# Kernel tuning notes

Hardware: AMD Instinct MI355X
Metric: run time of the kernel (lower is better)

The kernel has to match this reference:

```python
import jax, jax.numpy as jnp
import numpy as np

B = 524288   # batch of agents
N = 64       # neighbors (other agents)
H = 32       # hidden (hardcoded in original via zeros(1,32) and sqrt(32))
V = 256      # vocab_size
SCALE = np.float32(np.sqrt(32.0))  # original divides by sqrt(32) regardless of hidden


def setup_inputs() -> dict:
    key = jax.random.key(0)
    ks = jax.random.split(key, 24)
    lin = lambda k, i, o: (jax.random.normal(k, (i, o), jnp.float32) * (1.0 / np.sqrt(i)))
    inp = {
        'symbol': jax.random.randint(ks[0], (B,), 0, V, jnp.int32),
        'other_hidden': jax.random.normal(ks[1], (N, H), jnp.float32),
        'prev_hidden': jax.random.normal(ks[2], (B, H), jnp.float32),
        'emb': jax.random.normal(ks[3], (V, H), jnp.float32),
        'mem_gate': jnp.zeros((H,), jnp.float32),
        'Wm': lin(ks[4], H, H), 'bm': jnp.zeros((H,), jnp.float32),
        'Wq': lin(ks[5], H, H), 'bq': jnp.zeros((H,), jnp.float32),
        'Wk': lin(ks[6], H, H), 'bk': jnp.zeros((H,), jnp.float32),
        'Wv': lin(ks[7], H, H), 'bv': jnp.zeros((H,), jnp.float32),
        'W1': lin(ks[8], H, H), 'b1': jnp.zeros((H,), jnp.float32),
        'W2': lin(ks[9], H, H), 'b2': jnp.zeros((H,), jnp.float32),
        'W3': lin(ks[10], H, H), 'b3': jnp.zeros((H,), jnp.float32),
        'W4': lin(ks[11], H, H), 'b4': jnp.zeros((H,), jnp.float32),
        'Wa': lin(ks[12], H, 1), 'ba': jnp.zeros((1,), jnp.float32),
        'Ws': lin(ks[13], H, V), 'bs': jnp.zeros((V,), jnp.float32),
        'Wi': lin(ks[14], H, 3), 'bi': jnp.zeros((3,), jnp.float32),
    }
    return inp


def reference(symbol, other_hidden, prev_hidden, emb, mem_gate,
              Wm, bm, Wq, bq, Wk, bk, Wv, bv,
              W1, b1, W2, b2, W3, b3, W4, b4,
              Wa, ba, Ws, bs, Wi, bi):
    # embedding lookup
    h = emb[symbol]                                   # [B, H]
    # gated memory update
    gate = jax.nn.sigmoid(mem_gate)                   # [H]
    mem = jnp.tanh(prev_hidden @ Wm + bm)             # [B, H]
    h = h * (1.0 - gate) + mem * gate
    # social attention over shared neighbor set
    q = h @ Wq + bq                                   # [B, H]
    k = other_hidden @ Wk + bk                        # [N, H]
    v = other_hidden @ Wv + bv                        # [N, H]
    scores = (q @ k.T) / SCALE                        # [B, N]
    weights = jax.nn.softmax(scores, axis=-1)
    h = h + (weights @ v) * 0.3
    for W, b in ((W1, b1), (W2, b2), (W3, b3), (W4, b4)):
        h = h + jnp.tanh(h @ W + b) * 0.3
    # output heads
    action = jnp.tanh(h @ Wa + ba)                    # [B, 1]
    symbol_pred = h @ Ws + bs                         # [B, V]
    intent = h @ Wi + bi                              # [B, 3]
    return (action, symbol_pred, intent, h)
```

## Files before the change

kernel.cpp:

```cpp
#include <hip/hip_runtime.h>
#include <hip/hip_bf16.h>

constexpr int BTOT = 524288;
constexpr int NN   = 64;
constexpr int H    = 32;
constexpr int V    = 256;

typedef __attribute__((ext_vector_type(4))) float f32x4;
typedef __attribute__((ext_vector_type(4))) int   int4v;
typedef __attribute__((ext_vector_type(8))) short short8;

union FragU { int4v i; short8 s; };

__device__ __forceinline__ float fast_rcp(float x){ return __builtin_amdgcn_rcpf(x); }
__device__ __forceinline__ float fast_tanh(float x){
    float e = __expf(2.0f * x);
    return 1.0f - 2.0f * fast_rcp(e + 1.0f);
}
__device__ __forceinline__ int pkbf(float lo, float hi){
    union { __hip_bfloat162 h2; int i; } u;
    u.h2.x = __float2bfloat16(lo);
    u.h2.y = __float2bfloat16(hi);
    return u.i;
}
__device__ __forceinline__ void nt_store4(float* p, f32x4 v){
    __builtin_nontemporal_store(v, reinterpret_cast<f32x4*>(p));
}
__device__ __forceinline__ void nt_store1(float* p, float v){
    __builtin_nontemporal_store(v, p);
}

__device__ __attribute__((aligned(16))) int   g_Wfrag [6*2*64*4];
__device__ __attribute__((aligned(16))) int   g_Kfrag [4*64*4];
__device__ __attribute__((aligned(16))) int   g_Vfrag [2*2*64*4];
__device__ __attribute__((aligned(16))) int   g_Wsfrag[16*64*4];
__device__ __attribute__((aligned(16))) float g_biasd [6*64*8];
__device__ __attribute__((aligned(16))) float g_gated [64*8];
__device__ __attribute__((aligned(16))) float g_wad   [64*8];
__device__ __attribute__((aligned(16))) float g_wid   [64*24];

__global__ void precompute(const float* __restrict__ other_hidden,
                           const float* __restrict__ mem_gate,
                           const float* __restrict__ Wk, const float* __restrict__ bk,
                           const float* __restrict__ Wv, const float* __restrict__ bv,
                           const float* __restrict__ Wm, const float* __restrict__ bm,
                           const float* __restrict__ Wq, const float* __restrict__ bq,
                           const float* __restrict__ W1, const float* __restrict__ b1,
                           const float* __restrict__ W2, const float* __restrict__ b2,
                           const float* __restrict__ W3, const float* __restrict__ b3,
                           const float* __restrict__ W4, const float* __restrict__ b4,
                           const float* __restrict__ Wa, const float* __restrict__ Wi,
                           const float* __restrict__ Ws)
{
    __shared__ float Kst[64][32];
    __shared__ float Vst[64][32];
    __shared__ float gateS[32];
    const int t = threadIdx.x;

    if (t < 32) gateS[t] = fast_rcp(1.0f + __expf(-mem_gate[t]));
    {
        int n = t >> 2, c = (t & 3) * 8;
        float ak[8], av[8];
        #pragma unroll
        for (int i = 0; i < 8; ++i){ ak[i] = bk[c+i]; av[i] = bv[c+i]; }
        #pragma unroll
        for (int j = 0; j < H; ++j){
            float x = other_hidden[n*H + j];
            #pragma unroll
            for (int i = 0; i < 8; ++i){
                ak[i] = fmaf(x, Wk[j*H + c + i], ak[i]);
                av[i] = fmaf(x, Wv[j*H + c + i], av[i]);
            }
        }
        #pragma unroll
        for (int i = 0; i < 8; ++i){ Kst[n][c+i] = ak[i]; Vst[n][c+i] = av[i]; }
    }
    __syncthreads();

    #pragma unroll
    for (int w = 0; w < 6; ++w){
        const float* W = (w==0)?Wm : (w==1)?Wq : (w==2)?W1 : (w==3)?W2 : (w==4)?W3 : W4;
        for (int e = t; e < 128; e += 256){
            int mt = e >> 6, l = e & 63, la = l & 15, g = l >> 4;
            int m = mt*16 + la;
            int base = ((w*2 + mt)*64 + l)*4;
            #pragma unroll
            for (int j = 0; j < 4; ++j){
                int k0 = g*8 + 2*j;
                g_Wfrag[base + j] = pkbf(W[k0*H + m], W[(k0+1)*H + m]);
            }
        }
    }
    #pragma unroll
    for (int w = 0; w < 6; ++w){
        const float* bp_ = (w==0)?bm : (w==1)?bq : (w==2)?b1 : (w==3)?b2 : (w==4)?b3 : b4;
        for (int e = t; e < 512; e += 256){
            int l = e >> 3, idx = e & 7, mt = idx >> 2, r = idx & 3;
            int F = mt*16 + ((l>>4)&3)*4 + r;
            g_biasd[(w*64 + l)*8 + idx] = bp_[F];
        }
    }
    {
        int e = t;
        int mt = e >> 6, l = e & 63, la = l & 15, g = l >> 4;
        int n = mt*16 + la;
        #pragma unroll
        for (int j = 0; j < 4; ++j){
            int k0 = g*8 + 2*j;
            g_Kfrag[e*4 + j] = pkbf(Kst[n][k0], Kst[n][k0+1]);
        }
    }
    {
        int e = t;
        int mt = e >> 7, kt = (e >> 6) & 1, l = e & 63, la = l & 15, g = l >> 4;
        int m = mt*16 + la;
        #pragma unroll
        for (int j = 0; j < 4; ++j){
            int n0 = kt*32 + g*8 + 2*j;
            g_Vfrag[e*4 + j] = pkbf(Vst[n0][m], Vst[n0+1][m]);
        }
    }
    for (int e = t; e < 1024; e += 256){
        int mt = e >> 6, l = e & 63, la = l & 15, g = l >> 4;
        int m = mt*16 + la;
        #pragma unroll
        for (int j = 0; j < 4; ++j){
            int k0 = g*8 + 2*j;
            g_Wsfrag[e*4 + j] = pkbf(Ws[k0*V + m], Ws[(k0+1)*V + m]);
        }
    }
    for (int e = t; e < 512; e += 256){
        int l = e >> 3, idx = e & 7;
        int F = (idx>>2)*16 + ((l>>4)&3)*4 + (idx&3);
        g_gated[e] = gateS[F];
        g_wad[e]   = Wa[F];
    }
    for (int e = t; e < 1536; e += 256){
        int l = e / 24, m2 = e % 24, fidx = m2 / 3, j = m2 % 3;
        int F = (fidx>>2)*16 + ((l>>4)&3)*4 + (fidx&3);
        g_wid[e] = Wi[F*3 + j];
    }
}

__device__ __forceinline__ FragU d2b(f32x4 m0, f32x4 m1, int idxA, int idxB, bool glo){
    int p0a = pkbf(m0[0], m0[1]);
    int p1a = pkbf(m0[2], m0[3]);
    int p0b = pkbf(m1[0], m1[1]);
    int p1b = pkbf(m1[2], m1[3]);
    int tA0  = __builtin_amdgcn_ds_bpermute(idxA, p0a);
    int tA0b = __builtin_amdgcn_ds_bpermute(idxA, p0b);
    int tA1  = __builtin_amdgcn_ds_bpermute(idxA, p1a);
    int tA1b = __builtin_amdgcn_ds_bpermute(idxA, p1b);
    int tB0  = __builtin_amdgcn_ds_bpermute(idxB, p0a);
    int tB0b = __builtin_amdgcn_ds_bpermute(idxB, p0b);
    int tB1  = __builtin_amdgcn_ds_bpermute(idxB, p1a);
    int tB1b = __builtin_amdgcn_ds_bpermute(idxB, p1b);
    FragU r;
    r.i = int4v{ glo ? tA0 : tA0b, glo ? tA1 : tA1b,
                 glo ? tB0 : tB0b, glo ? tB1 : tB1b };
    return r;
}

__device__ __forceinline__ float bred_sum(float v, int bx16, int bx32){
    v += __int_as_float(__builtin_amdgcn_ds_bpermute(bx16, __float_as_int(v)));
    v += __int_as_float(__builtin_amdgcn_ds_bpermute(bx32, __float_as_int(v)));
    return v;
}
__device__ __forceinline__ float bred_max(float v, int bx16, int bx32){
    v = fmaxf(v, __int_as_float(__builtin_amdgcn_ds_bpermute(bx16, __float_as_int(v))));
    v = fmaxf(v, __int_as_float(__builtin_amdgcn_ds_bpermute(bx32, __float_as_int(v))));
    return v;
}
__device__ __forceinline__ f32x4 tanh4(f32x4 v){
    f32x4 r;
    r[0] = fast_tanh(v[0]); r[1] = fast_tanh(v[1]);
    r[2] = fast_tanh(v[2]); r[3] = fast_tanh(v[3]);
    return r;
}

#define MFMA(a, b, c) __builtin_amdgcn_mfma_f32_16x16x32_bf16((a), (b), (c), 0, 0, 0)

__global__ __launch_bounds__(256, 4) void social_main(
    const int*   __restrict__ symbol,
    const float* __restrict__ prev_hidden,
    const float* __restrict__ emb,
    const float* __restrict__ bs,
    const float* __restrict__ ba,
    const float* __restrict__ bi,
    float* __restrict__ out)
{
    const int tid = threadIdx.x;
    const int wv = tid >> 6, l = tid & 63;
    const int la = l & 15, g = l >> 4;
    const bool glo = (g < 2);
    const int idxA = (((g & 1) << 5) + la) << 2;
    const int idxB = idxA + 64;
    const int bx16 = (l ^ 16) << 2;
    const int bx32 = (l ^ 32) << 2;
    const int A0 = blockIdx.x * 128 + wv * 32;

    __shared__ f32x4 stgAll[4][256];
    __shared__ int4v sSF[1024];
    __shared__ float bsS[256];
    f32x4* buf = stgAll[wv];

    {
        const int4v* q4 = reinterpret_cast<const int4v*>(g_Wsfrag);
        for (int i = tid; i < 1024; i += 256) sSF[i] = q4[i];
        bsS[tid] = bs[tid];
    }
    __syncthreads();

    float* out_action = out;
    float* out_sym    = out + (size_t)BTOT;
    float* out_int    = out + (size_t)BTOT * (1 + V);
    float* out_h      = out + (size_t)BTOT * (1 + V + 3);

    const int4v* WF = reinterpret_cast<const int4v*>(g_Wfrag);
    const int4v* KF = reinterpret_cast<const int4v*>(g_Kfrag);
    const int4v* VF = reinterpret_cast<const int4v*>(g_Vfrag);
    const f32x4 zero4 = {0.f, 0.f, 0.f, 0.f};

    FragU phb[2];
    #pragma unroll
    for (int nt = 0; nt < 2; ++nt){
        const f32x4* p = reinterpret_cast<const f32x4*>(
            prev_hidden + (size_t)(A0 + nt*16 + la) * H + g*8);
        f32x4 v0 = p[0], v1 = p[1];
        phb[nt].i = int4v{ pkbf(v0[0],v0[1]), pkbf(v0[2],v0[3]),
                           pkbf(v1[0],v1[1]), pkbf(v1[2],v1[3]) };
    }

    f32x4 h_[2][2];
    {
        f32x4 bias[2];
        bias[0] = *reinterpret_cast<const f32x4*>(g_biasd + l*8);
        bias[1] = *reinterpret_cast<const f32x4*>(g_biasd + l*8 + 4);
        f32x4 m_[2][2];
        #pragma unroll
        for (int mt = 0; mt < 2; ++mt){
            FragU af; af.i = WF[(0*2 + mt)*64 + l];
            #pragma unroll
            for (int nt = 0; nt < 2; ++nt)
                m_[mt][nt] = MFMA(af.s, phb[nt].s, bias[mt]);
        }
        f32x4 gt[2];
        gt[0] = *reinterpret_cast<const f32x4*>(g_gated + l*8);
        gt[1] = *reinterpret_cast<const f32x4*>(g_gated + l*8 + 4);
        int sym0 = symbol[A0 + la], sym1 = symbol[A0 + 16 + la];
        #pragma unroll
        for (int mt = 0; mt < 2; ++mt)
        #pragma unroll
        for (int nt = 0; nt < 2; ++nt){
            const float* eb = emb + (size_t)(nt ? sym1 : sym0)*H + mt*16 + g*4;
            #pragma unroll
            for (int r = 0; r < 4; ++r){
                float gv = gt[mt][r];
                h_[mt][nt][r] = eb[r]*(1.0f - gv) + fast_tanh(m_[mt][nt][r])*gv;
            }
        }
    }

    f32x4 q_[2][2];
    {
        f32x4 bias[2];
        bias[0] = *reinterpret_cast<const f32x4*>(g_biasd + 512 + l*8);
        bias[1] = *reinterpret_cast<const f32x4*>(g_biasd + 512 + l*8 + 4);
        FragU hb[2] = { d2b(h_[0][0], h_[1][0], idxA, idxB, glo),
                        d2b(h_[0][1], h_[1][1], idxA, idxB, glo) };
        #pragma unroll
        for (int mt = 0; mt < 2; ++mt){
            FragU af; af.i = WF[(1*2 + mt)*64 + l];
            #pragma unroll
            for (int nt = 0; nt < 2; ++nt)
                q_[mt][nt] = MFMA(af.s, hb[nt].s, bias[mt]);
        }
    }

    f32x4 s_[4][2];
    {
        FragU qb[2] = { d2b(q_[0][0], q_[1][0], idxA, idxB, glo),
                        d2b(q_[0][1], q_[1][1], idxA, idxB, glo) };
        #pragma unroll
        for (int mt = 0; mt < 4; ++mt){
            FragU af; af.i = KF[mt*64 + l];
            #pragma unroll
            for (int nt = 0; nt < 2; ++nt)
                s_[mt][nt] = MFMA(af.s, qb[nt].s, zero4);
        }
    }

    const float INVS = 0.17677669529663687f;
    float coef[2];
    #pragma unroll
    for (int nt = 0; nt < 2; ++nt){
        float mx = s_[0][nt][0];
        #pragma unroll
        for (int mt = 0; mt < 4; ++mt)
        #pragma unroll
        for (int r = 0; r < 4; ++r) mx = fmaxf(mx, s_[mt][nt][r]);
        mx = bred_max(mx, bx16, bx32);
        float den = 0.f;
        #pragma unroll
        for (int mt = 0; mt < 4; ++mt)
        #pragma unroll
        for (int r = 0; r < 4; ++r){
            float w = __expf((s_[mt][nt][r] - mx) * INVS);
            s_[mt][nt][r] = w;
            den += w;
        }
        den = bred_sum(den, bx16, bx32);
        coef[nt] = 0.3f * fast_rcp(den);
    }

    {
        FragU wb[2][2];
        #pragma unroll
        for (int kt = 0; kt < 2; ++kt)
        #pragma unroll
        for (int nt = 0; nt < 2; ++nt)
            wb[kt][nt] = d2b(s_[2*kt][nt], s_[2*kt+1][nt], idxA, idxB, glo);
        #pragma unroll
        for (int mt = 0; mt < 2; ++mt){
            FragU vf0, vf1;
            vf0.i = VF[(mt*2 + 0)*64 + l];
            vf1.i = VF[(mt*2 + 1)*64 + l];
            #pragma unroll
            for (int nt = 0; nt < 2; ++nt){
                f32x4 acc = MFMA(vf0.s, wb[0][nt].s, zero4);
                acc = MFMA(vf1.s, wb[1][nt].s, acc);
                h_[mt][nt] += acc * coef[nt];
            }
        }
    }

    for (int blk = 0; blk < 4; ++blk){
        f32x4 bias[2];
        bias[0] = *reinterpret_cast<const f32x4*>(g_biasd + (2+blk)*512 + l*8);
        bias[1] = *reinterpret_cast<const f32x4*>(g_biasd + (2+blk)*512 + l*8 + 4);
        FragU hb[2] = { d2b(h_[0][0], h_[1][0], idxA, idxB, glo),
                        d2b(h_[0][1], h_[1][1], idxA, idxB, glo) };
        #pragma unroll
        for (int mt = 0; mt < 2; ++mt){
            FragU af; af.i = WF[((2+blk)*2 + mt)*64 + l];
            #pragma unroll
            for (int nt = 0; nt < 2; ++nt){
                f32x4 tv = MFMA(af.s, hb[nt].s, bias[mt]);
                h_[mt][nt] += 0.3f * tanh4(tv);
            }
        }
    }

    FragU hb[2] = { d2b(h_[0][0], h_[1][0], idxA, idxB, glo),
                    d2b(h_[0][1], h_[1][1], idxA, idxB, glo) };

    {
        union { f32x4 v[2]; float s[8]; } wa;
        wa.v[0] = *reinterpret_cast<const f32x4*>(g_wad + l*8);
        wa.v[1] = *reinterpret_cast<const f32x4*>(g_wad + l*8 + 4);
        float ba0 = ba[0];
        float act[2];
        #pragma unroll
        for (int nt = 0; nt < 2; ++nt){
            float acc = 0.f;
            #pragma unroll
            for (int mt = 0; mt < 2; ++mt)
            #pragma unroll
            for (int r = 0; r < 4; ++r)
                acc = fmaf(h_[mt][nt][r], wa.s[mt*4 + r], acc);
            acc = bred_sum(acc, bx16, bx32);
            act[nt] = fast_tanh(acc + ba0);
        }
        if (l < 16){
            nt_store1(out_action + A0 + la,      act[0]);
            nt_store1(out_action + A0 + 16 + la, act[1]);
        }
    }

    {
        union { f32x4 v[6]; float s[24]; } wi;
        #pragma unroll
        for (int k = 0; k < 6; ++k)
            wi.v[k] = *(reinterpret_cast<const f32x4*>(g_wid + l*24) + k);
        float bi0 = bi[0], bi1 = bi[1], bi2 = bi[2];
        #pragma unroll
        for (int nt = 0; nt < 2; ++nt){
            float i0 = 0.f, i1 = 0.f, i2 = 0.f;
            #pragma unroll
            for (int mt = 0; mt < 2; ++mt)
            #pragma unroll
            for (int r = 0; r < 4; ++r){
                float hv = h_[mt][nt][r];
                int base = (mt*4 + r)*3;
                i0 = fmaf(hv, wi.s[base + 0], i0);
                i1 = fmaf(hv, wi.s[base + 1], i1);
                i2 = fmaf(hv, wi.s[base + 2], i2);
            }
            i0 = bred_sum(i0, bx16, bx32) + bi0;
            i1 = bred_sum(i1, bx16, bx32) + bi1;
            i2 = bred_sum(i2, bx16, bx32) + bi2;
            if (l < 16){
                size_t a = (size_t)(A0 + nt*16 + la);
                nt_store1(out_int + a*3 + 0, i0);
                nt_store1(out_int + a*3 + 1, i1);
                nt_store1(out_int + a*3 + 2, i2);
            }
        }
    }

    {
        #pragma unroll
        for (int nt = 0; nt < 2; ++nt)
        #pragma unroll
        for (int mt = 0; mt < 2; ++mt){
            int a = nt*16 + la;
            int blk = mt*4 + g;
            buf[a*8 + (blk ^ (a & 7))] = h_[mt][nt];
        }
        int rdA = l >> 3, rdB = l & 7;
        #pragma unroll
        for (int j = 0; j < 4; ++j){
            int a = j*8 + rdA;
            f32x4 ov = buf[a*8 + (rdB ^ (a & 7))];
            nt_store4(out_h + (size_t)(A0 + a)*H + rdB*4, ov);
        }
    }

    {
        int rdA = l >> 3, rdB = l & 7;
        #pragma unroll
        for (int mtp = 0; mtp < 8; ++mtp){
            #pragma unroll
            for (int hh = 0; hh < 2; ++hh){
                int mt = mtp*2 + hh;
                FragU af; af.i = sSF[mt*64 + l];
                f32x4 o0 = MFMA(af.s, hb[0].s, zero4);
                f32x4 o1 = MFMA(af.s, hb[1].s, zero4);
                int blk = hh*4 + g;
                int a0 = la, a1 = 16 + la;
                buf[a0*8 + (blk ^ (a0 & 7))] = o0;
                buf[a1*8 + (blk ^ (a1 & 7))] = o1;
            }
            f32x4 bv = *reinterpret_cast<const f32x4*>(bsS + mtp*32 + rdB*4);
            #pragma unroll
            for (int j = 0; j < 4; ++j){
                int a = j*8 + rdA;
                f32x4 ov = buf[a*8 + (rdB ^ (a & 7))];
                ov += bv;
                nt_store4(out_sym + (size_t)(A0 + a)*V + mtp*32 + rdB*4, ov);
            }
        }
    }
}

extern "C" void kernel_launch(void* const* d_in, const int* in_sizes, int n_in,
                              void* d_out, int out_size, void* d_ws, size_t ws_size,
                              hipStream_t stream)
{
    const int*   symbol       = (const int*)  d_in[0];
    const float* other_hidden = (const float*)d_in[1];
    const float* prev_hidden  = (const float*)d_in[2];
    const float* emb          = (const float*)d_in[3];
    const float* mem_gate     = (const float*)d_in[4];
    const float* Wm  = (const float*)d_in[5];  const float* bm = (const float*)d_in[6];
    const float* Wq  = (const float*)d_in[7];  const float* bq = (const float*)d_in[8];
    const float* Wk  = (const float*)d_in[9];  const float* bk = (const float*)d_in[10];
    const float* Wv  = (const float*)d_in[11]; const float* bv = (const float*)d_in[12];
    const float* W1  = (const float*)d_in[13]; const float* b1 = (const float*)d_in[14];
    const float* W2  = (const float*)d_in[15]; const float* b2 = (const float*)d_in[16];
    const float* W3  = (const float*)d_in[17]; const float* b3 = (const float*)d_in[18];
    const float* W4  = (const float*)d_in[19]; const float* b4 = (const float*)d_in[20];
    const float* Wa  = (const float*)d_in[21]; const float* ba = (const float*)d_in[22];
    const float* Wsm = (const float*)d_in[23]; const float* bs = (const float*)d_in[24];
    const float* Wi  = (const float*)d_in[25]; const float* bi = (const float*)d_in[26];

    precompute<<<1, 256, 0, stream>>>(other_hidden, mem_gate, Wk, bk, Wv, bv,
                                      Wm, bm, Wq, bq, W1, b1, W2, b2, W3, b3, W4, b4,
                                      Wa, Wi, Wsm);

    social_main<<<BTOT / 128, 256, 0, stream>>>(symbol, prev_hidden, emb, bs, ba, bi,
                                                (float*)d_out);
}
```

Baseline: 137.3 us.

## Process two agent tiles per wave with software-prefetched inputs

Each block now handles 256 agents by looping over two 32-agent tiles per wave. Prefetching the second tile's prev_hidden, symbols and embedding rows during the first tile's compute hides global-load latency, and the per-block LDS setup of Ws fragments and bs is amortized over twice as many agents. Launch bounds drop to 2 blocks per SM to allow more registers for the prefetched state. This halves the grid and may reduce occupancy.

```diff
diff --git a/kernel.cpp b/kernel.cpp
--- a/kernel.cpp
+++ b/kernel.cpp
@@ -180,7 +180,7 @@
 
 #define MFMA(a, b, c) __builtin_amdgcn_mfma_f32_16x16x32_bf16((a), (b), (c), 0, 0, 0)
 
-__global__ __launch_bounds__(256, 4) void social_main(
+__global__ __launch_bounds__(256, 2) void social_main(
     const int*   __restrict__ symbol,
     const float* __restrict__ prev_hidden,
     const float* __restrict__ emb,
@@ -197,7 +197,7 @@
     const int idxB = idxA + 64;
     const int bx16 = (l ^ 16) << 2;
     const int bx32 = (l ^ 32) << 2;
-    const int A0 = blockIdx.x * 128 + wv * 32;
+    const int base = blockIdx.x * 256 + wv * 32;
 
     __shared__ f32x4 stgAll[4][256];
     __shared__ int4v sSF[1024];
@@ -221,233 +221,273 @@
     const int4v* VF = reinterpret_cast<const int4v*>(g_Vfrag);
     const f32x4 zero4 = {0.f, 0.f, 0.f, 0.f};
 
-    FragU phb[2];
+    FragU phbA[2][2];
+    f32x4 emA[2][2][2];
+    int symN0, symN1;
+
+    {
+        #pragma unroll
+        for (int nt = 0; nt < 2; ++nt){
+            const f32x4* p = reinterpret_cast<const f32x4*>(
+                prev_hidden + (size_t)(base + nt*16 + la) * H + g*8);
+            f32x4 v0 = p[0], v1 = p[1];
+            phbA[0][nt].i = int4v{ pkbf(v0[0],v0[1]), pkbf(v0[2],v0[3]),
+                                   pkbf(v1[0],v1[1]), pkbf(v1[2],v1[3]) };
+        }
+        int s0 = symbol[base + la], s1 = symbol[base + 16 + la];
+        symN0 = symbol[base + 128 + la];
+        symN1 = symbol[base + 128 + 16 + la];
+        #pragma unroll
+        for (int mt = 0; mt < 2; ++mt)
+        #pragma unroll
+        for (int nt = 0; nt < 2; ++nt)
+            emA[0][mt][nt] = *reinterpret_cast<const f32x4*>(
+                emb + (size_t)(nt ? s1 : s0)*H + mt*16 + g*4);
+    }
+
     #pragma unroll
-    for (int nt = 0; nt < 2; ++nt){
-        const f32x4* p = reinterpret_cast<const f32x4*>(
-            prev_hidden + (size_t)(A0 + nt*16 + la) * H + g*8);
-        f32x4 v0 = p[0], v1 = p[1];
-        phb[nt].i = int4v{ pkbf(v0[0],v0[1]), pkbf(v0[2],v0[3]),
-                           pkbf(v1[0],v1[1]), pkbf(v1[2],v1[3]) };
-    }
-
-    f32x4 h_[2][2];
-    {
-        f32x4 bias[2];
-        bias[0] = *reinterpret_cast<const f32x4*>(g_biasd + l*8);
-        bias[1] = *reinterpret_cast<const f32x4*>(g_biasd + l*8 + 4);
-        f32x4 m_[2][2];
-        #pragma unroll
-        for (int mt = 0; mt < 2; ++mt){
-            FragU af; af.i = WF[(0*2 + mt)*64 + l];
+    for (int t = 0; t < 2; ++t){
+        const int A0 = base + t*128;
+
+        f32x4 pvr[2][2];
+        if (t == 0){
+            #pragma unroll
+            for (int nt = 0; nt < 2; ++nt){
+                const f32x4* p = reinterpret_cast<const f32x4*>(
+                    prev_hidden + (size_t)(base + 128 + nt*16 + la) * H + g*8);
+                pvr[nt][0] = p[0]; pvr[nt][1] = p[1];
+            }
+        }
+
+        f32x4 h_[2][2];
+        {
+            f32x4 bias0 = *reinterpret_cast<const f32x4*>(g_biasd + l*8);
+            f32x4 bias1 = *reinterpret_cast<const f32x4*>(g_biasd + l*8 + 4);
+            f32x4 m_[2][2];
+            #pragma unroll
+            for (int mt = 0; mt < 2; ++mt){
+                FragU af; af.i = WF[(0*2 + mt)*64 + l];
+                #pragma unroll
+                for (int nt = 0; nt < 2; ++nt)
+                    m_[mt][nt] = MFMA(af.s, phbA[t][nt].s, mt ? bias1 : bias0);
+            }
+            f32x4 gt0 = *reinterpret_cast<const f32x4*>(g_gated + l*8);
+            f32x4 gt1 = *reinterpret_cast<const f32x4*>(g_gated + l*8 + 4);
+            #pragma unroll
+            for (int mt = 0; mt < 2; ++mt)
+            #pragma unroll
+            for (int nt = 0; nt < 2; ++nt){
+                #pragma unroll
+                for (int r = 0; r < 4; ++r){
+                    float gv = mt ? gt1[r] : gt0[r];
+                    h_[mt][nt][r] = emA[t][mt][nt][r]*(1.0f - gv)
+                                  + fast_tanh(m_[mt][nt][r])*gv;
+                }
+            }
+        }
+
+        f32x4 q_[2][2];
+        {
+            f32x4 bias0 = *reinterpret_cast<const f32x4*>(g_biasd + 512 + l*8);
+            f32x4 bias1 = *reinterpret_cast<const f32x4*>(g_biasd + 512 + l*8 + 4);
+            FragU hb0[2] = { d2b(h_[0][0], h_[1][0], idxA, idxB, glo),
+                             d2b(h_[0][1], h_[1][1], idxA, idxB, glo) };
+            #pragma unroll
+            for (int mt = 0; mt < 2; ++mt){
+                FragU af; af.i = WF[(1*2 + mt)*64 + l];
+                #pragma unroll
+                for (int nt = 0; nt < 2; ++nt)
+                    q_[mt][nt] = MFMA(af.s, hb0[nt].s, mt ? bias1 : bias0);
+            }
+        }
+
+        f32x4 s_[4][2];
+        {
+            FragU qb[2] = { d2b(q_[0][0], q_[1][0], idxA, idxB, glo),
+                            d2b(q_[0][1], q_[1][1], idxA, idxB, glo) };
+            #pragma unroll
+            for (int mt = 0; mt < 4; ++mt){
+                FragU af; af.i = KF[mt*64 + l];
+                #pragma unroll
+                for (int nt = 0; nt < 2; ++nt)
+                    s_[mt][nt] = MFMA(af.s, qb[nt].s, zero4);
+            }
+        }
+
+        if (t == 0){
+            #pragma unroll
+            for (int mt = 0; mt < 2; ++mt)
             #pragma unroll
             for (int nt = 0; nt < 2; ++nt)
-                m_[mt][nt] = MFMA(af.s, phb[nt].s, bias[mt]);
-        }
-        f32x4 gt[2];
-        gt[0] = *reinterpret_cast<const f32x4*>(g_gated + l*8);
-        gt[1] = *reinterpret_cast<const f32x4*>(g_gated + l*8 + 4);
-        int sym0 = symbol[A0 + la], sym1 = symbol[A0 + 16 + la];
-        #pragma unroll
-        for (int mt = 0; mt < 2; ++mt)
+                emA[1][mt][nt] = *reinterpret_cast<const f32x4*>(
+                    emb + (size_t)(nt ? symN1 : symN0)*H + mt*16 + g*4);
+            #pragma unroll
+            for (int nt = 0; nt < 2; ++nt)
+                phbA[1][nt].i = int4v{ pkbf(pvr[nt][0][0], pvr[nt][0][1]),
+                                       pkbf(pvr[nt][0][2], pvr[nt][0][3]),
+                                       pkbf(pvr[nt][1][0], pvr[nt][1][1]),
+                                       pkbf(pvr[nt][1][2], pvr[nt][1][3]) };
+        }
+
+        const float INVS = 0.17677669529663687f;
+        float coef[2];
         #pragma unroll
         for (int nt = 0; nt < 2; ++nt){
-            const float* eb = emb + (size_t)(nt ? sym1 : sym0)*H + mt*16 + g*4;
+            float mx = s_[0][nt][0];
+            #pragma unroll
+            for (int mt = 0; mt < 4; ++mt)
+            #pragma unroll
+            for (int r = 0; r < 4; ++r) mx = fmaxf(mx, s_[mt][nt][r]);
+            mx = bred_max(mx, bx16, bx32);
+            float den = 0.f;
+            #pragma unroll
+            for (int mt = 0; mt < 4; ++mt)
             #pragma unroll
             for (int r = 0; r < 4; ++r){
-                float gv = gt[mt][r];
-                h_[mt][nt][r] = eb[r]*(1.0f - gv) + fast_tanh(m_[mt][nt][r])*gv;
-            }
-        }
-    }
-
-    f32x4 q_[2][2];
-    {
-        f32x4 bias[2];
-        bias[0] = *reinterpret_cast<const f32x4*>(g_biasd + 512 + l*8);
-        bias[1] = *reinterpret_cast<const f32x4*>(g_biasd + 512 + l*8 + 4);
+                float w = __expf((s_[mt][nt][r] - mx) * INVS);
+                s_[mt][nt][r] = w;
+                den += w;
+            }
+            den = bred_sum(den, bx16, bx32);
+            coef[nt] = 0.3f * fast_rcp(den);
+        }
+
+        {
+            FragU wb[2][2];
+            #pragma unroll
+            for (int kt = 0; kt < 2; ++kt)
+            #pragma unroll
+            for (int nt = 0; nt < 2; ++nt)
+                wb[kt][nt] = d2b(s_[2*kt][nt], s_[2*kt+1][nt], idxA, idxB, glo);
+            #pragma unroll
+            for (int mt = 0; mt < 2; ++mt){
+                FragU vf0, vf1;
+                vf0.i = VF[(mt*2 + 0)*64 + l];
+                vf1.i = VF[(mt*2 + 1)*64 + l];
+                #pragma unroll
+                for (int nt = 0; nt < 2; ++nt){
+                    f32x4 acc = MFMA(vf0.s, wb[0][nt].s, zero4);
+                    acc = MFMA(vf1.s, wb[1][nt].s, acc);
+                    h_[mt][nt] += acc * coef[nt];
+                }
+            }
+        }
+
+        #pragma unroll 1
+        for (int blk = 0; blk < 4; ++blk){
+            f32x4 bias0 = *reinterpret_cast<const f32x4*>(g_biasd + (2+blk)*512 + l*8);
+            f32x4 bias1 = *reinterpret_cast<const f32x4*>(g_biasd + (2+blk)*512 + l*8 + 4);
+            FragU hb1[2] = { d2b(h_[0][0], h_[1][0], idxA, idxB, glo),
+                             d2b(h_[0][1], h_[1][1], idxA, idxB, glo) };
+            #pragma unroll
+            for (int mt = 0; mt < 2; ++mt){
+                FragU af; af.i = WF[((2+blk)*2 + mt)*64 + l];
+                #pragma unroll
+                for (int nt = 0; nt < 2; ++nt){
+                    f32x4 tv = MFMA(af.s, hb1[nt].s, mt ? bias1 : bias0);
+                    h_[mt][nt] += 0.3f * tanh4(tv);
+                }
+            }
+        }
+
         FragU hb[2] = { d2b(h_[0][0], h_[1][0], idxA, idxB, glo),
                         d2b(h_[0][1], h_[1][1], idxA, idxB, glo) };
-        #pragma unroll
-        for (int mt = 0; mt < 2; ++mt){
-            FragU af; af.i = WF[(1*2 + mt)*64 + l];
+
+        {
+            union { f32x4 v[2]; float s[8]; } wa;
+            wa.v[0] = *reinterpret_cast<const f32x4*>(g_wad + l*8);
+            wa.v[1] = *reinterpret_cast<const f32x4*>(g_wad + l*8 + 4);
+            float ba0 = ba[0];
+            float act[2];
+            #pragma unroll
+            for (int nt = 0; nt < 2; ++nt){
+                float acc = 0.f;
+                #pragma unroll
+                for (int mt = 0; mt < 2; ++mt)
+                #pragma unroll
+                for (int r = 0; r < 4; ++r)
+                    acc = fmaf(h_[mt][nt][r], wa.s[mt*4 + r], acc);
+                acc = bred_sum(acc, bx16, bx32);
+                act[nt] = fast_tanh(acc + ba0);
+            }
+            if (l < 16){
+                nt_store1(out_action + A0 + la,      act[0]);
+                nt_store1(out_action + A0 + 16 + la, act[1]);
+            }
+        }
+
+        {
+            union { f32x4 v[6]; float s[24]; } wi;
+            #pragma unroll
+            for (int k = 0; k < 6; ++k)
+                wi.v[k] = *(reinterpret_cast<const f32x4*>(g_wid + l*24) + k);
+            float bi0 = bi[0], bi1 = bi[1], bi2 = bi[2];
+            #pragma unroll
+            for (int nt = 0; nt < 2; ++nt){
+                float i0 = 0.f, i1 = 0.f, i2 = 0.f;
+                #pragma unroll
+                for (int mt = 0; mt < 2; ++mt)
+                #pragma unroll
+                for (int r = 0; r < 4; ++r){
+                    float hv = h_[mt][nt][r];
+                    int bidx = (mt*4 + r)*3;
+                    i0 = fmaf(hv, wi.s[bidx + 0], i0);
+                    i1 = fmaf(hv, wi.s[bidx + 1], i1);
+                    i2 = fmaf(hv, wi.s[bidx + 2], i2);
+                }
+                i0 = bred_sum(i0, bx16, bx32) + bi0;
+                i1 = bred_sum(i1, bx16, bx32) + bi1;
+                i2 = bred_sum(i2, bx16, bx32) + bi2;
+                if (l < 16){
+                    size_t a = (size_t)(A0 + nt*16 + la);
+                    nt_store1(out_int + a*3 + 0, i0);
+                    nt_store1(out_int + a*3 + 1, i1);
+                    nt_store1(out_int + a*3 + 2, i2);
+                }
+            }
+        }
+
+        {
             #pragma unroll
             for (int nt = 0; nt < 2; ++nt)
-                q_[mt][nt] = MFMA(af.s, hb[nt].s, bias[mt]);
-        }
-    }
-
-    f32x4 s_[4][2];
-    {
-        FragU qb[2] = { d2b(q_[0][0], q_[1][0], idxA, idxB, glo),
-                        d2b(q_[0][1], q_[1][1], idxA, idxB, glo) };
-        #pragma unroll
-        for (int mt = 0; mt < 4; ++mt){
-            FragU af; af.i = KF[mt*64 + l];
-            #pragma unroll
-            for (int nt = 0; nt < 2; ++nt)
-                s_[mt][nt] = MFMA(af.s, qb[nt].s, zero4);
-        }
-    }
-
-    const float INVS = 0.17677669529663687f;
-    float coef[2];
-    #pragma unroll
-    for (int nt = 0; nt < 2; ++nt){
-        float mx = s_[0][nt][0];
-        #pragma unroll
-        for (int mt = 0; mt < 4; ++mt)
-        #pragma unroll
-        for (int r = 0; r < 4; ++r) mx = fmaxf(mx, s_[mt][nt][r]);
-        mx = bred_max(mx, bx16, bx32);
-        float den = 0.f;
-        #pragma unroll
-        for (int mt = 0; mt < 4; ++mt)
-        #pragma unroll
-        for (int r = 0; r < 4; ++r){
-            float w = __expf((s_[mt][nt][r] - mx) * INVS);
-            s_[mt][nt][r] = w;
-            den += w;
-        }
-        den = bred_sum(den, bx16, bx32);
-        coef[nt] = 0.3f * fast_rcp(den);
-    }
-
-    {
-        FragU wb[2][2];
-        #pragma unroll
-        for (int kt = 0; kt < 2; ++kt)
-        #pragma unroll
-        for (int nt = 0; nt < 2; ++nt)
-            wb[kt][nt] = d2b(s_[2*kt][nt], s_[2*kt+1][nt], idxA, idxB, glo);
-        #pragma unroll
-        for (int mt = 0; mt < 2; ++mt){
-            FragU vf0, vf1;
-            vf0.i = VF[(mt*2 + 0)*64 + l];
-            vf1.i = VF[(mt*2 + 1)*64 + l];
-            #pragma unroll
-            for (int nt = 0; nt < 2; ++nt){
-                f32x4 acc = MFMA(vf0.s, wb[0][nt].s, zero4);
-                acc = MFMA(vf1.s, wb[1][nt].s, acc);
-                h_[mt][nt] += acc * coef[nt];
-            }
-        }
-    }
-
-    for (int blk = 0; blk < 4; ++blk){
-        f32x4 bias[2];
-        bias[0] = *reinterpret_cast<const f32x4*>(g_biasd + (2+blk)*512 + l*8);
-        bias[1] = *reinterpret_cast<const f32x4*>(g_biasd + (2+blk)*512 + l*8 + 4);
-        FragU hb[2] = { d2b(h_[0][0], h_[1][0], idxA, idxB, glo),
-                        d2b(h_[0][1], h_[1][1], idxA, idxB, glo) };
-        #pragma unroll
-        for (int mt = 0; mt < 2; ++mt){
-            FragU af; af.i = WF[((2+blk)*2 + mt)*64 + l];
-            #pragma unroll
-            for (int nt = 0; nt < 2; ++nt){
-                f32x4 tv = MFMA(af.s, hb[nt].s, bias[mt]);
-                h_[mt][nt] += 0.3f * tanh4(tv);
-            }
-        }
-    }
-
-    FragU hb[2] = { d2b(h_[0][0], h_[1][0], idxA, idxB, glo),
-                    d2b(h_[0][1], h_[1][1], idxA, idxB, glo) };
-
-    {
-        union { f32x4 v[2]; float s[8]; } wa;
-        wa.v[0] = *reinterpret_cast<const f32x4*>(g_wad + l*8);
-        wa.v[1] = *reinterpret_cast<const f32x4*>(g_wad + l*8 + 4);
-        float ba0 = ba[0];
-        float act[2];
-        #pragma unroll
-        for (int nt = 0; nt < 2; ++nt){
-            float acc = 0.f;
-            #pragma unroll
-            for (int mt = 0; mt < 2; ++mt)
-            #pragma unroll
-            for (int r = 0; r < 4; ++r)
-                acc = fmaf(h_[mt][nt][r], wa.s[mt*4 + r], acc);
-            acc = bred_sum(acc, bx16, bx32);
-            act[nt] = fast_tanh(acc + ba0);
-        }
-        if (l < 16){
-            nt_store1(out_action + A0 + la,      act[0]);
-            nt_store1(out_action + A0 + 16 + la, act[1]);
-        }
-    }
-
-    {
-        union { f32x4 v[6]; float s[24]; } wi;
-        #pragma unroll
-        for (int k = 0; k < 6; ++k)
-            wi.v[k] = *(reinterpret_cast<const f32x4*>(g_wid + l*24) + k);
-        float bi0 = bi[0], bi1 = bi[1], bi2 = bi[2];
-        #pragma unroll
-        for (int nt = 0; nt < 2; ++nt){
-            float i0 = 0.f, i1 = 0.f, i2 = 0.f;
-            #pragma unroll
-            for (int mt = 0; mt < 2; ++mt)
-            #pragma unroll
-            for (int r = 0; r < 4; ++r){
-                float hv = h_[mt][nt][r];
-                int base = (mt*4 + r)*3;
-                i0 = fmaf(hv, wi.s[base + 0], i0);
-                i1 = fmaf(hv, wi.s[base + 1], i1);
-                i2 = fmaf(hv, wi.s[base + 2], i2);
-            }
-            i0 = bred_sum(i0, bx16, bx32) + bi0;
-            i1 = bred_sum(i1, bx16, bx32) + bi1;
-            i2 = bred_sum(i2, bx16, bx32) + bi2;
-            if (l < 16){
-                size_t a = (size_t)(A0 + nt*16 + la);
-                nt_store1(out_int + a*3 + 0, i0);
-                nt_store1(out_int + a*3 + 1, i1);
-                nt_store1(out_int + a*3 + 2, i2);
-            }
-        }
-    }
-
-    {
-        #pragma unroll
-        for (int nt = 0; nt < 2; ++nt)
-        #pragma unroll
-        for (int mt = 0; mt < 2; ++mt){
-            int a = nt*16 + la;
-            int blk = mt*4 + g;
-            buf[a*8 + (blk ^ (a & 7))] = h_[mt][nt];
-        }
-        int rdA = l >> 3, rdB = l & 7;
-        #pragma unroll
-        for (int j = 0; j < 4; ++j){
-            int a = j*8 + rdA;
-            f32x4 ov = buf[a*8 + (rdB ^ (a & 7))];
-            nt_store4(out_h + (size_t)(A0 + a)*H + rdB*4, ov);
-        }
-    }
-
-    {
-        int rdA = l >> 3, rdB = l & 7;
-        #pragma unroll
-        for (int mtp = 0; mtp < 8; ++mtp){
-            #pragma unroll
-            for (int hh = 0; hh < 2; ++hh){
-                int mt = mtp*2 + hh;
-                FragU af; af.i = sSF[mt*64 + l];
-                f32x4 o0 = MFMA(af.s, hb[0].s, zero4);
-                f32x4 o1 = MFMA(af.s, hb[1].s, zero4);
-                int blk = hh*4 + g;
-                int a0 = la, a1 = 16 + la;
-                buf[a0*8 + (blk ^ (a0 & 7))] = o0;
-                buf[a1*8 + (blk ^ (a1 & 7))] = o1;
-            }
-            f32x4 bv = *reinterpret_cast<const f32x4*>(bsS + mtp*32 + rdB*4);
+            #pragma unroll
+            for (int mt = 0; mt < 2; ++mt){
+                int a = nt*16 + la;
+                int blk = mt*4 + g;
+                buf[a*8 + (blk ^ (a & 7))] = h_[mt][nt];
+            }
+            int rdA = l >> 3, rdB = l & 7;
             #pragma unroll
             for (int j = 0; j < 4; ++j){
                 int a = j*8 + rdA;
                 f32x4 ov = buf[a*8 + (rdB ^ (a & 7))];
-                ov += bv;
-                nt_store4(out_sym + (size_t)(A0 + a)*V + mtp*32 + rdB*4, ov);
+                nt_store4(out_h + (size_t)(A0 + a)*H + rdB*4, ov);
+            }
+        }
+
+        {
+            int rdA = l >> 3, rdB = l & 7;
+            #pragma unroll
+            for (int mtp = 0; mtp < 8; ++mtp){
+                #pragma unroll
+                for (int hh = 0; hh < 2; ++hh){
+                    int mt = mtp*2 + hh;
+                    FragU af; af.i = sSF[mt*64 + l];
+                    f32x4 o0 = MFMA(af.s, hb[0].s, zero4);
+                    f32x4 o1 = MFMA(af.s, hb[1].s, zero4);
+                    int blk = hh*4 + g;
+                    int a0 = la, a1 = 16 + la;
+                    buf[a0*8 + (blk ^ (a0 & 7))] = o0;
+                    buf[a1*8 + (blk ^ (a1 & 7))] = o1;
+                }
+                f32x4 bv = *reinterpret_cast<const f32x4*>(bsS + mtp*32 + rdB*4);
+                #pragma unroll
+                for (int j = 0; j < 4; ++j){
+                    int a = j*8 + rdA;
+                    f32x4 ov = buf[a*8 + (rdB ^ (a & 7))];
+                    ov += bv;
+                    nt_store4(out_sym + (size_t)(A0 + a)*V + mtp*32 + rdB*4, ov);
+                }
             }
         }
     }
@@ -478,6 +518,6 @@
                                       Wm, bm, Wq, bq, W1, b1, W2, b2, W3, b3, W4, b4,
                                       Wa, Wi, Wsm);
 
-    social_main<<<BTOT / 128, 256, 0, stream>>>(symbol, prev_hidden, emb, bs, ba, bi,
+    social_main<<<BTOT / 256, 256, 0, stream>>>(symbol, prev_hidden, emb, bs, ba, bi,
                                                 (float*)d_out);
 }
```

Result: faster. 132.9 us, median of 2 (-3.2%).
